# Kernel tuning notes

Measured on AMD Instinct MI355X. Metric: run time of the kernel, lower is better.

Reference implementation:

```python
import jax, jax.numpy as jnp
import numpy as np
from jax import lax

FAN_IN = 16          # fixed number of parents per decoder node
THRESHOLD = 12       # node is active iff >= 12/16 parents are active
K_NODES = 1024       # decoders in this layer
M_PREV = 1024        # nodes in previous layer
N_SPATIAL = 64       # n x n output matrices


def setup_inputs() -> dict:
    key = jax.random.key(0)
    k1, k2, k3, k4, k5 = jax.random.split(key, 5)
    prev_outputs = jax.random.normal(k1, (M_PREV, N_SPATIAL, N_SPATIAL), dtype=jnp.float32)
    # Bernoulli(0.85) so the 12/16 threshold gate is genuinely data-dependent
    prev_is_active = jax.random.bernoulli(k2, 0.85, (M_PREV,))
    parent_indices = jax.random.randint(k3, (K_NODES, FAN_IN), 0, M_PREV, dtype=jnp.int32)
    # Per-node decoder params: 3x3 conv collapsing 16 parent channels -> 1 map, plus bias
    W = jax.random.normal(k4, (K_NODES, FAN_IN, 3, 3), dtype=jnp.float32) * 0.05
    b = jax.random.normal(k5, (K_NODES,), dtype=jnp.float32) * 0.05
    return {"prev_outputs": prev_outputs, "prev_is_active": prev_is_active,
            "parent_indices": parent_indices, "W": W, "b": b}


def reference(prev_outputs, prev_is_active, parent_indices, W, b):
    K, n = parent_indices.shape[0], prev_outputs.shape[-1]
    # Irregular static-wiring gather: (K, 16, n, n) and (K, 16)
    gathered = prev_outputs[parent_indices]
    gathered_flags = prev_is_active[parent_indices]
    # Threshold gate: node active iff >= 12 of its 16 parents are active
    out_active = jnp.sum(gathered_flags.astype(jnp.int32), axis=1) >= THRESHOLD  # (K,)
    # K independent 16->1 convs with distinct weights == one grouped conv (groups = K)
    x = gathered.reshape(1, K * FAN_IN, n, n)          # NCHW
    y = lax.conv_general_dilated(
        x, W, window_strides=(1, 1), padding='SAME',
        dimension_numbers=('NCHW', 'OIHW', 'NCHW'),
        feature_group_count=K,
    )[0]                                               # (K, n, n)
    y = jnp.tanh(y + b[:, None, None])
    # Inactive nodes emit a zero tensor
    out = jnp.where(out_active[:, None, None], y, jnp.zeros((), dtype=y.dtype))
    return out, out_active
```

## Files before the change

### kernel.cpp

```cpp
#include <hip/hip_runtime.h>

#define KN      1024
#define FAN_IN  16
#define NSP     64
#define MAPB    (NSP * NSP)
#define THRESH  12

__device__ __forceinline__ float tanh_fast(float x) {
    float ax = fabsf(x);
    float e  = __expf(-2.0f * ax);
    float r  = 1.0f - 2.0f * e * __builtin_amdgcn_rcpf(1.0f + e);
    return copysignf(r, x);
}

__device__ __forceinline__ float dpp_wshr1(float x) {
    return __int_as_float(__builtin_amdgcn_update_dpp(
        0, __float_as_int(x), 0x138, 0xF, 0xF, true));
}
__device__ __forceinline__ float dpp_wshl1(float x) {
    return __int_as_float(__builtin_amdgcn_update_dpp(
        0, __float_as_int(x), 0x130, 0xF, 0xF, true));
}

__device__ __forceinline__ unsigned short f2bf_rne(float x) {
    unsigned u = __float_as_uint(x);
    return (unsigned short)((u + 0x7FFFu + ((u >> 16) & 1u)) >> 16);
}
__device__ __forceinline__ float bf2f(unsigned short s) {
    return __uint_as_float(((unsigned)s) << 16);
}

__global__ __launch_bounds__(256) void compress_kernel(
    const float* __restrict__ in, unsigned short* __restrict__ out16)
{
    const int i = (blockIdx.x * 256 + threadIdx.x) * 4;
    float4 v = *(const float4*)(in + i);
    ushort4 o;
    o.x = f2bf_rne(v.x); o.y = f2bf_rne(v.y);
    o.z = f2bf_rne(v.z); o.w = f2bf_rne(v.w);
    *(ushort4*)(out16 + i) = o;
}

__global__ __launch_bounds__(512, 8) void decoder_bf16(
    const unsigned short* __restrict__ maps16,
    const void*  __restrict__ prev_is_active,
    const int*   __restrict__ parent_indices,
    const float* __restrict__ Wt,
    const float* __restrict__ bias,
    float*       __restrict__ out)
{
    __shared__ unsigned short sbuf[2][MAPB];

    const int k    = blockIdx.x;
    const int tid  = threadIdx.x;
    const int lane = tid & 63;
    const int wv   = tid >> 6;
    const int r0   = wv * 8;

    bool bytemode = false;
    {
        const unsigned* sv = (const unsigned*)prev_is_active;
        #pragma unroll
        for (int i = 0; i < 16; ++i)
            if (sv[i] > 1u) bytemode = true;
    }

    const int* pidx = parent_indices + k * FAN_IN;
    int cnt = 0;
    #pragma unroll
    for (int i = 0; i < FAN_IN; ++i) {
        int p = pidx[i];
        int f;
        if (bytemode) f = (((const unsigned char*)prev_is_active)[p] != 0);
        else          f = (((const int*)prev_is_active)[p] != 0);
        cnt += f;
    }
    const bool active = (cnt >= THRESH);

    const size_t obase = (size_t)k * MAPB;
    if (tid == 0)
        out[(size_t)KN * MAPB + k] = active ? 1.0f : 0.0f;

    if (!active) {
        float4 z = make_float4(0.f, 0.f, 0.f, 0.f);
        float4* o4 = (float4*)(out + obase);
        o4[tid]       = z;
        o4[tid + 512] = z;
        return;
    }

    const float mT = (wv > 0) ? 1.0f : 0.0f;
    const float mB = (wv < 7) ? 1.0f : 0.0f;
    const int   rT = (wv > 0) ? r0 - 1 : 0;
    const int   rB = (wv < 7) ? r0 + 8 : 63;

    const float* wbase = Wt + (size_t)k * FAN_IN * 9;

    float acc[8];
    #pragma unroll
    for (int s = 0; s < 8; ++s) acc[s] = 0.0f;

#define STAGE(buf, p)                                                          \
    __builtin_amdgcn_global_load_lds(                                          \
        (const __attribute__((address_space(1))) unsigned*)                    \
            ((const char*)maps16 + (size_t)(p) * 8192 + tid * 16),             \
        (__attribute__((address_space(3))) unsigned*)                          \
            ((char*)&sbuf[buf][0] + wv * 1024),                                \
        16, 0, 0);

    STAGE(0, pidx[0]);
    __syncthreads();

    #pragma unroll 2
    for (int ch = 0; ch < FAN_IN; ++ch) {
        if (ch + 1 < FAN_IN) STAGE((ch + 1) & 1, pidx[ch + 1]);

        const unsigned short* sb = sbuf[ch & 1];
        const float* w = wbase + ch * 9;
        const float wl0 = w[0], wc0 = w[1], wr0 = w[2];
        const float wl1 = w[3], wc1 = w[4], wr1 = w[5];
        const float wl2 = w[6], wc2 = w[7], wr2 = w[8];

        float v[10], l[10], r[10];
        v[0] = bf2f(sb[rT * NSP + lane]) * mT;
        #pragma unroll
        for (int j = 1; j <= 8; ++j) v[j] = bf2f(sb[(r0 - 1 + j) * NSP + lane]);
        v[9] = bf2f(sb[rB * NSP + lane]) * mB;
        #pragma unroll
        for (int j = 0; j < 10; ++j) { l[j] = dpp_wshr1(v[j]); r[j] = dpp_wshl1(v[j]); }

        #pragma unroll
        for (int s = 0; s < 8; ++s) {
            float a = acc[s];
            a = fmaf(wl0, l[s],     fmaf(wc0, v[s],     fmaf(wr0, r[s],     a)));
            a = fmaf(wl1, l[s + 1], fmaf(wc1, v[s + 1], fmaf(wr1, r[s + 1], a)));
            a = fmaf(wl2, l[s + 2], fmaf(wc2, v[s + 2], fmaf(wr2, r[s + 2], a)));
            acc[s] = a;
        }

        if (ch + 1 < FAN_IN) __syncthreads();
    }
#undef STAGE

    const float bk = bias[k];
    #pragma unroll
    for (int s = 0; s < 8; ++s)
        out[obase + (size_t)(r0 + s) * NSP + lane] = tanh_fast(acc[s] + bk);
}

__device__ __forceinline__ void gload_lds16f(const float* g, float* l) {
    __builtin_amdgcn_global_load_lds(
        (const __attribute__((address_space(1))) unsigned*)g,
        (__attribute__((address_space(3)))       unsigned*)l,
        16, 0, 0);
}

__global__ __launch_bounds__(512, 8) void decoder_f32(
    const float* __restrict__ prev_outputs,
    const void*  __restrict__ prev_is_active,
    const int*   __restrict__ parent_indices,
    const float* __restrict__ Wt,
    const float* __restrict__ bias,
    float*       __restrict__ out)
{
    __shared__ float sbuf[2][MAPB];

    const int k    = blockIdx.x;
    const int tid  = threadIdx.x;
    const int lane = tid & 63;
    const int wv   = tid >> 6;
    const int r0   = wv * 8;

    bool bytemode = false;
    {
        const unsigned* sv = (const unsigned*)prev_is_active;
        #pragma unroll
        for (int i = 0; i < 16; ++i)
            if (sv[i] > 1u) bytemode = true;
    }

    const int* pidx = parent_indices + k * FAN_IN;
    int cnt = 0;
    #pragma unroll
    for (int i = 0; i < FAN_IN; ++i) {
        int p = pidx[i];
        int f;
        if (bytemode) f = (((const unsigned char*)prev_is_active)[p] != 0);
        else          f = (((const int*)prev_is_active)[p] != 0);
        cnt += f;
    }
    const bool active = (cnt >= THRESH);

    const size_t obase = (size_t)k * MAPB;
    if (tid == 0)
        out[(size_t)KN * MAPB + k] = active ? 1.0f : 0.0f;

    if (!active) {
        float4 z = make_float4(0.f, 0.f, 0.f, 0.f);
        float4* o4 = (float4*)(out + obase);
        o4[tid]       = z;
        o4[tid + 512] = z;
        return;
    }

    const float mT = (wv > 0) ? 1.0f : 0.0f;
    const float mB = (wv < 7) ? 1.0f : 0.0f;
    const int   rT = (wv > 0) ? r0 - 1 : 0;
    const int   rB = (wv < 7) ? r0 + 8 : 63;

    const float* wbase = Wt + (size_t)k * FAN_IN * 9;

    float acc[8];
    #pragma unroll
    for (int s = 0; s < 8; ++s) acc[s] = 0.0f;

#define STAGE(buf, p)                                                         \
    {                                                                         \
        const float* g = prev_outputs + (size_t)(p) * MAPB;                   \
        gload_lds16f(g + tid * 4,        &sbuf[buf][wv * 256]);               \
        gload_lds16f(g + 2048 + tid * 4, &sbuf[buf][2048 + wv * 256]);        \
    }

    STAGE(0, pidx[0]);
    __syncthreads();

    #pragma unroll 2
    for (int ch = 0; ch < FAN_IN; ++ch) {
        if (ch + 1 < FAN_IN) STAGE((ch + 1) & 1, pidx[ch + 1]);

        const float* sb = sbuf[ch & 1];
        const float* w  = wbase + ch * 9;
        const float wl0 = w[0], wc0 = w[1], wr0 = w[2];
        const float wl1 = w[3], wc1 = w[4], wr1 = w[5];
        const float wl2 = w[6], wc2 = w[7], wr2 = w[8];

        float v[10], l[10], r[10];
        v[0] = sb[rT * NSP + lane] * mT;
        #pragma unroll
        for (int j = 1; j <= 8; ++j) v[j] = sb[(r0 - 1 + j) * NSP + lane];
        v[9] = sb[rB * NSP + lane] * mB;
        #pragma unroll
        for (int j = 0; j < 10; ++j) { l[j] = dpp_wshr1(v[j]); r[j] = dpp_wshl1(v[j]); }

        #pragma unroll
        for (int s = 0; s < 8; ++s) {
            float a = acc[s];
            a = fmaf(wl0, l[s],     fmaf(wc0, v[s],     fmaf(wr0, r[s],     a)));
            a = fmaf(wl1, l[s + 1], fmaf(wc1, v[s + 1], fmaf(wr1, r[s + 1], a)));
            a = fmaf(wl2, l[s + 2], fmaf(wc2, v[s + 2], fmaf(wr2, r[s + 2], a)));
            acc[s] = a;
        }

        if (ch + 1 < FAN_IN) __syncthreads();
    }
#undef STAGE

    const float bk = bias[k];
    #pragma unroll
    for (int s = 0; s < 8; ++s)
        out[obase + (size_t)(r0 + s) * NSP + lane] = tanh_fast(acc[s] + bk);
}

extern "C" void kernel_launch(void* const* d_in, const int* in_sizes, int n_in,
                              void* d_out, int out_size, void* d_ws, size_t ws_size,
                              hipStream_t stream) {
    const float* prev_outputs   = (const float*)d_in[0];
    const void*  prev_is_active = d_in[1];
    const int*   parent_indices = (const int*)d_in[2];
    const float* Wt             = (const float*)d_in[3];
    const float* bias           = (const float*)d_in[4];
    float*       out            = (float*)d_out;

    const size_t need = (size_t)KN * MAPB * sizeof(unsigned short);
    if (ws_size >= need) {
        unsigned short* maps16 = (unsigned short*)d_ws;
        compress_kernel<<<dim3(KN * MAPB / (256 * 4)), dim3(256), 0, stream>>>(
            prev_outputs, maps16);
        decoder_bf16<<<dim3(KN), dim3(512), 0, stream>>>(
            maps16, prev_is_active, parent_indices, Wt, bias, out);
    } else {
        decoder_f32<<<dim3(KN), dim3(512), 0, stream>>>(
            prev_outputs, prev_is_active, parent_indices, Wt, bias, out);
    }
}
```

Before: 42.19 us.

## Split each decoder node across two half-map blocks with halo row loads

The bf16 decoder now launches two 256-thread blocks per node, each computing 32 rows of the 64x64 output. Each block stages only its half of every parent map into LDS and fetches the one boundary halo row with direct global loads, which are software-pipelined one channel ahead. The goal is more blocks and smaller LDS use, giving better CU occupancy and load balance. The costs are duplicated gate computation and weight loads per node, plus extra uncoalesced halo loads.

```diff
diff --git a/kernel.cpp b/kernel.cpp
--- a/kernel.cpp
+++ b/kernel.cpp
@@ -41,7 +41,7 @@
     *(ushort4*)(out16 + i) = o;
 }
 
-__global__ __launch_bounds__(512, 8) void decoder_bf16(
+__global__ __launch_bounds__(256) void decoder_bf16(
     const unsigned short* __restrict__ maps16,
     const void*  __restrict__ prev_is_active,
     const int*   __restrict__ parent_indices,
@@ -49,13 +49,15 @@
     const float* __restrict__ bias,
     float*       __restrict__ out)
 {
-    __shared__ unsigned short sbuf[2][MAPB];
-
-    const int k    = blockIdx.x;
+    __shared__ unsigned short sbuf[2][32 * NSP];
+
+    const int bid  = blockIdx.x;
+    const int k    = bid >> 1;
+    const int h    = bid & 1;
     const int tid  = threadIdx.x;
     const int lane = tid & 63;
     const int wv   = tid >> 6;
-    const int r0   = wv * 8;
+    const int r0   = h * 32 + wv * 8;
 
     bool bytemode = false;
     {
@@ -78,21 +80,21 @@
     const bool active = (cnt >= THRESH);
 
     const size_t obase = (size_t)k * MAPB;
-    if (tid == 0)
+    if (h == 0 && tid == 0)
         out[(size_t)KN * MAPB + k] = active ? 1.0f : 0.0f;
 
     if (!active) {
         float4 z = make_float4(0.f, 0.f, 0.f, 0.f);
-        float4* o4 = (float4*)(out + obase);
+        float4* o4 = (float4*)(out + obase + (size_t)h * 32 * NSP);
         o4[tid]       = z;
-        o4[tid + 512] = z;
+        o4[tid + 256] = z;
         return;
     }
 
-    const float mT = (wv > 0) ? 1.0f : 0.0f;
-    const float mB = (wv < 7) ? 1.0f : 0.0f;
-    const int   rT = (wv > 0) ? r0 - 1 : 0;
-    const int   rB = (wv < 7) ? r0 + 8 : 63;
+    const float mT = (h == 1) ? 1.0f : 0.0f;
+    const float mB = (h == 0) ? 1.0f : 0.0f;
+    const int   haloTrow = (h == 1) ? 31 : 0;
+    const int   haloBrow = (h == 0) ? 32 : 63;
 
     const float* wbase = Wt + (size_t)k * FAN_IN * 9;
 
@@ -100,20 +102,28 @@
     #pragma unroll
     for (int s = 0; s < 8; ++s) acc[s] = 0.0f;
 
-#define STAGE(buf, p)                                                          \
-    __builtin_amdgcn_global_load_lds(                                          \
-        (const __attribute__((address_space(1))) unsigned*)                    \
-            ((const char*)maps16 + (size_t)(p) * 8192 + tid * 16),             \
-        (__attribute__((address_space(3))) unsigned*)                          \
-            ((char*)&sbuf[buf][0] + wv * 1024),                                \
-        16, 0, 0);
-
-    STAGE(0, pidx[0]);
+    unsigned short hT_n, hB_n;
+
+#define STAGE(b, ch)                                                          \
+    {                                                                         \
+        const size_t pb = (size_t)pidx[ch] * MAPB;                            \
+        __builtin_amdgcn_global_load_lds(                                     \
+            (const __attribute__((address_space(1))) unsigned*)               \
+                ((const char*)maps16 + pb * 2 + h * 4096 + tid * 16),         \
+            (__attribute__((address_space(3))) unsigned*)                     \
+                ((char*)&sbuf[b][0] + wv * 1024),                             \
+            16, 0, 0);                                                        \
+        hT_n = maps16[pb + haloTrow * NSP + lane];                            \
+        hB_n = maps16[pb + haloBrow * NSP + lane];                            \
+    }
+
+    STAGE(0, 0);
     __syncthreads();
 
     #pragma unroll 2
     for (int ch = 0; ch < FAN_IN; ++ch) {
-        if (ch + 1 < FAN_IN) STAGE((ch + 1) & 1, pidx[ch + 1]);
+        const unsigned short hT = hT_n, hB = hB_n;
+        if (ch + 1 < FAN_IN) STAGE((ch + 1) & 1, ch + 1);
 
         const unsigned short* sb = sbuf[ch & 1];
         const float* w = wbase + ch * 9;
@@ -121,11 +131,13 @@
         const float wl1 = w[3], wc1 = w[4], wr1 = w[5];
         const float wl2 = w[6], wc2 = w[7], wr2 = w[8];
 
+        const int lT = (wv > 0) ? wv * 8 - 1 : 0;
+        const int lB = (wv < 3) ? wv * 8 + 8 : 31;
         float v[10], l[10], r[10];
-        v[0] = bf2f(sb[rT * NSP + lane]) * mT;
-        #pragma unroll
-        for (int j = 1; j <= 8; ++j) v[j] = bf2f(sb[(r0 - 1 + j) * NSP + lane]);
-        v[9] = bf2f(sb[rB * NSP + lane]) * mB;
+        v[0] = (wv == 0) ? bf2f(hT) * mT : bf2f(sb[lT * NSP + lane]);
+        #pragma unroll
+        for (int j = 1; j <= 8; ++j) v[j] = bf2f(sb[(wv * 8 - 1 + j) * NSP + lane]);
+        v[9] = (wv == 3) ? bf2f(hB) * mB : bf2f(sb[lB * NSP + lane]);
         #pragma unroll
         for (int j = 0; j < 10; ++j) { l[j] = dpp_wshr1(v[j]); r[j] = dpp_wshl1(v[j]); }
 
@@ -214,19 +226,19 @@
     #pragma unroll
     for (int s = 0; s < 8; ++s) acc[s] = 0.0f;
 
-#define STAGE(buf, p)                                                         \
+#define STAGE(b, ch)                                                          \
     {                                                                         \
-        const float* g = prev_outputs + (size_t)(p) * MAPB;                   \
-        gload_lds16f(g + tid * 4,        &sbuf[buf][wv * 256]);               \
-        gload_lds16f(g + 2048 + tid * 4, &sbuf[buf][2048 + wv * 256]);        \
-    }
-
-    STAGE(0, pidx[0]);
+        const float* g = prev_outputs + (size_t)pidx[ch] * MAPB;              \
+        gload_lds16f(g + tid * 4,        &sbuf[b][wv * 256]);                 \
+        gload_lds16f(g + 2048 + tid * 4, &sbuf[b][2048 + wv * 256]);          \
+    }
+
+    STAGE(0, 0);
     __syncthreads();
 
     #pragma unroll 2
     for (int ch = 0; ch < FAN_IN; ++ch) {
-        if (ch + 1 < FAN_IN) STAGE((ch + 1) & 1, pidx[ch + 1]);
+        if (ch + 1 < FAN_IN) STAGE((ch + 1) & 1, ch + 1);
 
         const float* sb = sbuf[ch & 1];
         const float* w  = wbase + ch * 9;
@@ -276,7 +288,7 @@
         unsigned short* maps16 = (unsigned short*)d_ws;
         compress_kernel<<<dim3(KN * MAPB / (256 * 4)), dim3(256), 0, stream>>>(
             prev_outputs, maps16);
-        decoder_bf16<<<dim3(KN), dim3(512), 0, stream>>>(
+        decoder_bf16<<<dim3(KN * 2), dim3(256), 0, stream>>>(
             maps16, prev_is_active, parent_indices, Wt, bias, out);
     } else {
         decoder_f32<<<dim3(KN), dim3(512), 0, stream>>>(
```

Result: slower. 47.54 us (+12.7%).

## Deepen bf16 decoder LDS pipeline to 8 stages with explicit vmcnt waits

Applied to the files above, without the earlier changes.

Replaces the double-buffered LDS staging in the bf16 decoder with an 8-slot ring buffer. It prefetches 7 parent maps ahead, fully unrolls the 16 channels, and uses explicit s_waitcnt vmcnt plus a raw barrier per phase. The goal is to keep more global->LDS loads in flight and hide memory latency. The cost is 64KB of LDS per block and a dropped occupancy hint, which lowers the number of resident blocks per CU. The f32 path only has its STAGE macro reworked and otherwise keeps its double buffer.

```diff
diff --git a/kernel.cpp b/kernel.cpp
--- a/kernel.cpp
+++ b/kernel.cpp
@@ -41,7 +41,7 @@
     *(ushort4*)(out16 + i) = o;
 }
 
-__global__ __launch_bounds__(512, 8) void decoder_bf16(
+__global__ __launch_bounds__(512) void decoder_bf16(
     const unsigned short* __restrict__ maps16,
     const void*  __restrict__ prev_is_active,
     const int*   __restrict__ parent_indices,
@@ -49,7 +49,7 @@
     const float* __restrict__ bias,
     float*       __restrict__ out)
 {
-    __shared__ unsigned short sbuf[2][MAPB];
+    __shared__ unsigned short sbuf[8][MAPB];
 
     const int k    = blockIdx.x;
     const int tid  = threadIdx.x;
@@ -100,46 +100,57 @@
     #pragma unroll
     for (int s = 0; s < 8; ++s) acc[s] = 0.0f;
 
-#define STAGE(buf, p)                                                          \
-    __builtin_amdgcn_global_load_lds(                                          \
-        (const __attribute__((address_space(1))) unsigned*)                    \
-            ((const char*)maps16 + (size_t)(p) * 8192 + tid * 16),             \
-        (__attribute__((address_space(3))) unsigned*)                          \
-            ((char*)&sbuf[buf][0] + wv * 1024),                                \
+#define STAGE(b, ch)                                                          \
+    __builtin_amdgcn_global_load_lds(                                         \
+        (const __attribute__((address_space(1))) unsigned*)                   \
+            ((const char*)maps16 + (size_t)pidx[ch] * 8192 + tid * 16),       \
+        (__attribute__((address_space(3))) unsigned*)                         \
+            ((char*)&sbuf[b][0] + wv * 1024),                                 \
         16, 0, 0);
 
-    STAGE(0, pidx[0]);
-    __syncthreads();
-
-    #pragma unroll 2
-    for (int ch = 0; ch < FAN_IN; ++ch) {
-        if (ch + 1 < FAN_IN) STAGE((ch + 1) & 1, pidx[ch + 1]);
-
-        const unsigned short* sb = sbuf[ch & 1];
-        const float* w = wbase + ch * 9;
-        const float wl0 = w[0], wc0 = w[1], wr0 = w[2];
-        const float wl1 = w[3], wc1 = w[4], wr1 = w[5];
-        const float wl2 = w[6], wc2 = w[7], wr2 = w[8];
-
-        float v[10], l[10], r[10];
-        v[0] = bf2f(sb[rT * NSP + lane]) * mT;
-        #pragma unroll
-        for (int j = 1; j <= 8; ++j) v[j] = bf2f(sb[(r0 - 1 + j) * NSP + lane]);
-        v[9] = bf2f(sb[rB * NSP + lane]) * mB;
-        #pragma unroll
-        for (int j = 0; j < 10; ++j) { l[j] = dpp_wshr1(v[j]); r[j] = dpp_wshl1(v[j]); }
-
-        #pragma unroll
-        for (int s = 0; s < 8; ++s) {
-            float a = acc[s];
-            a = fmaf(wl0, l[s],     fmaf(wc0, v[s],     fmaf(wr0, r[s],     a)));
-            a = fmaf(wl1, l[s + 1], fmaf(wc1, v[s + 1], fmaf(wr1, r[s + 1], a)));
-            a = fmaf(wl2, l[s + 2], fmaf(wc2, v[s + 2], fmaf(wr2, r[s + 2], a)));
-            acc[s] = a;
-        }
-
-        if (ch + 1 < FAN_IN) __syncthreads();
-    }
+#define COMPUTE(ch)                                                           \
+    {                                                                         \
+        const unsigned short* sb = sbuf[(ch) & 7];                            \
+        const float* w = wbase + (ch) * 9;                                    \
+        const float wl0 = w[0], wc0 = w[1], wr0 = w[2];                       \
+        const float wl1 = w[3], wc1 = w[4], wr1 = w[5];                       \
+        const float wl2 = w[6], wc2 = w[7], wr2 = w[8];                       \
+        float v[10], l[10], r[10];                                            \
+        v[0] = bf2f(sb[rT * NSP + lane]) * mT;                                \
+        _Pragma("unroll")                                                     \
+        for (int j = 1; j <= 8; ++j) v[j] = bf2f(sb[(r0 - 1 + j) * NSP + lane]); \
+        v[9] = bf2f(sb[rB * NSP + lane]) * mB;                                \
+        _Pragma("unroll")                                                     \
+        for (int j = 0; j < 10; ++j) { l[j] = dpp_wshr1(v[j]); r[j] = dpp_wshl1(v[j]); } \
+        _Pragma("unroll")                                                     \
+        for (int s = 0; s < 8; ++s) {                                         \
+            float a = acc[s];                                                 \
+            a = fmaf(wl0, l[s],     fmaf(wc0, v[s],     fmaf(wr0, r[s],     a))); \
+            a = fmaf(wl1, l[s + 1], fmaf(wc1, v[s + 1], fmaf(wr1, r[s + 1], a))); \
+            a = fmaf(wl2, l[s + 2], fmaf(wc2, v[s + 2], fmaf(wr2, r[s + 2], a))); \
+            acc[s] = a;                                                       \
+        }                                                                     \
+    }
+
+#define PHASE(ch, N)                                                          \
+    asm volatile("s_waitcnt vmcnt(" #N ")" ::: "memory");                     \
+    __builtin_amdgcn_s_barrier();                                             \
+    __builtin_amdgcn_sched_barrier(0);                                        \
+    if ((ch) + 7 < FAN_IN) { STAGE(((ch) + 7) & 7, (ch) + 7); }               \
+    COMPUTE(ch)
+
+    asm volatile("s_waitcnt vmcnt(0)" ::: "memory");
+
+    STAGE(0, 0); STAGE(1, 1); STAGE(2, 2); STAGE(3, 3);
+    STAGE(4, 4); STAGE(5, 5); STAGE(6, 6);
+
+    PHASE(0, 6);   PHASE(1, 6);   PHASE(2, 6);   PHASE(3, 6);
+    PHASE(4, 6);   PHASE(5, 6);   PHASE(6, 6);   PHASE(7, 6);
+    PHASE(8, 6);   PHASE(9, 6);   PHASE(10, 5);  PHASE(11, 4);
+    PHASE(12, 3);  PHASE(13, 2);  PHASE(14, 1);  PHASE(15, 0);
+
+#undef PHASE
+#undef COMPUTE
 #undef STAGE
 
     const float bk = bias[k];
@@ -214,19 +225,19 @@
     #pragma unroll
     for (int s = 0; s < 8; ++s) acc[s] = 0.0f;
 
-#define STAGE(buf, p)                                                         \
+#define STAGE(b, ch)                                                          \
     {                                                                         \
-        const float* g = prev_outputs + (size_t)(p) * MAPB;                   \
-        gload_lds16f(g + tid * 4,        &sbuf[buf][wv * 256]);               \
-        gload_lds16f(g + 2048 + tid * 4, &sbuf[buf][2048 + wv * 256]);        \
-    }
-
-    STAGE(0, pidx[0]);
+        const float* g = prev_outputs + (size_t)pidx[ch] * MAPB;              \
+        gload_lds16f(g + tid * 4,        &sbuf[b][wv * 256]);                 \
+        gload_lds16f(g + 2048 + tid * 4, &sbuf[b][2048 + wv * 256]);          \
+    }
+
+    STAGE(0, 0);
     __syncthreads();
 
     #pragma unroll 2
     for (int ch = 0; ch < FAN_IN; ++ch) {
-        if (ch + 1 < FAN_IN) STAGE((ch + 1) & 1, pidx[ch + 1]);
+        if (ch + 1 < FAN_IN) STAGE((ch + 1) & 1, ch + 1);
 
         const float* sb = sbuf[ch & 1];
         const float* w  = wbase + ch * 9;
```

Result: slower. 51.49 us (+22.1%).
